# Kernel tuning notes

Hardware: AMD Instinct MI355X
Metric: run time of the kernel (lower is better)

The kernel has to match this reference:

```python
import jax, jax.numpy as jnp
import numpy as np

N_NODES = 10000
N_PAIRS = 200000
NUM_FEATURES = 384
DEGREES = [1, 2, 3]
NHEADS = len(DEGREES)
F_HEAD = NUM_FEATURES // NHEADS  # 128
REPEATS = np.array([2 * d + 1 for d in DEGREES])  # [3,5,7]
SPH_DIM = int(REPEATS.sum())  # 15


def setup_inputs() -> dict:
    key = jax.random.key(0)
    ks = jax.random.split(key, 10)
    return {
        "chi": jax.random.normal(ks[0], (N_NODES, SPH_DIM), dtype=jnp.float32),
        "sph_ij": jax.random.normal(ks[1], (N_PAIRS, SPH_DIM), dtype=jnp.float32),
        "x": jax.random.normal(ks[2], (N_NODES, NUM_FEATURES), dtype=jnp.float32),
        "w_ij": jax.random.normal(ks[3], (N_PAIRS, NUM_FEATURES), dtype=jnp.float32),
        "idx_i": jax.random.randint(ks[4], (N_PAIRS,), 0, N_NODES),
        "phi_r_cut": jax.random.uniform(ks[5], (N_PAIRS, 1), dtype=jnp.float32),
        "phi_chi_cut": jax.random.uniform(ks[6], (N_PAIRS,), dtype=jnp.float32),
        "idx_j": jax.random.randint(ks[7], (N_PAIRS,), 0, N_NODES),
        # per-head linear weights (nn.Linear stores (out, in); y = x @ W.T)
        "Wq": jax.random.normal(ks[8], (NHEADS, F_HEAD, F_HEAD), dtype=jnp.float32) / np.sqrt(F_HEAD),
        "Wk": jax.random.normal(ks[9], (NHEADS, F_HEAD, F_HEAD), dtype=jnp.float32) / np.sqrt(F_HEAD),
    }


def reference(chi, sph_ij, x, w_ij, idx_i, phi_r_cut, phi_chi_cut, idx_j, Wq, Wk):
    n = x.shape[0]
    # split into heads: (n, H, Fh) / (E, H, Fh)
    x_h = x.reshape(n, NHEADS, F_HEAD)
    w_h = w_ij.reshape(-1, NHEADS, F_HEAD)
    # per-head linears (vmapped Linear, no bias): y = x @ W.T
    q = jnp.einsum("nhf,hgf->nhg", x_h, Wq)  # (n, H, Fh)
    k = jnp.einsum("nhf,hgf->nhg", x_h, Wk)  # (n, H, Fh)
    # gather + elementwise attention coefficients per head: (E, H)
    alpha = (q[idx_i] * w_h * k[idx_j]).sum(-1) / np.sqrt(F_HEAD).astype(np.float32)
    # combine radial and sphc cutoffs
    alpha = alpha * phi_r_cut + alpha * phi_chi_cut[:, None]  # (E, H)
    # repeat each head over its 2l+1 spherical components -> (E, SPH_DIM)
    alpha_rep = jnp.repeat(alpha, REPEATS, axis=-1, total_repeat_length=SPH_DIM)
    # scatter-add messages into center atoms -> (n, SPH_DIM)
    chi_ = jax.ops.segment_sum(alpha_rep * sph_ij, idx_i, num_segments=n)
    return chi_
```

## Files before the change

kernel.cpp:

```cpp
#include <hip/hip_runtime.h>
#include <hip/hip_bf16.h>
#include <hip/hip_fp16.h>

#define N_NODES 10000
#define N_PAIRS 200000
#define NFEAT 384
#define FH 128
#define SPH 15

typedef __bf16 bf16x8 __attribute__((ext_vector_type(8)));
typedef _Float16 half8 __attribute__((ext_vector_type(8)));
typedef float f32x4 __attribute__((ext_vector_type(4)));

__device__ inline bf16x8 cvt8(const float* __restrict__ p) {
    float4 lo = *(const float4*)p;
    float4 hi = *(const float4*)(p + 4);
    bf16x8 r;
    r[0] = (__bf16)lo.x; r[1] = (__bf16)lo.y; r[2] = (__bf16)lo.z; r[3] = (__bf16)lo.w;
    r[4] = (__bf16)hi.x; r[5] = (__bf16)hi.y; r[6] = (__bf16)hi.z; r[7] = (__bf16)hi.w;
    return r;
}

__global__ __launch_bounds__(256) void qk_gemm_kernel(
        const float* __restrict__ x,
        const float* __restrict__ Wq,
        const float* __restrict__ Wk,
        _Float16* __restrict__ q, _Float16* __restrict__ k) {
    const int head = blockIdx.y;
    const int node0 = blockIdx.x * 16;
    const int wave = threadIdx.x >> 6;
    const int lane = threadIdx.x & 63;
    const int mrow = lane & 15;
    const int quad = lane >> 4;
    const float* xrow = x + (size_t)(node0 + mrow) * NFEAT + head * FH + quad * 8;
    bf16x8 afrag[4];
#pragma unroll
    for (int t = 0; t < 4; ++t) afrag[t] = cvt8(xrow + t * 32);

    for (int task = wave; task < 16; task += 4) {
        const int mat = task & 1;
        const int g0 = (task >> 1) * 16;
        const float* Wrow =
            (mat ? Wk : Wq) + (size_t)head * FH * FH + (size_t)(g0 + mrow) * FH + quad * 8;
        f32x4 acc = {0.f, 0.f, 0.f, 0.f};
#pragma unroll
        for (int t = 0; t < 4; ++t) {
            bf16x8 b = cvt8(Wrow + t * 32);
            acc = __builtin_amdgcn_mfma_f32_16x16x32_bf16(afrag[t], b, acc, 0, 0, 0);
        }
        _Float16* dst = mat ? k : q;
        const int g = g0 + mrow;
#pragma unroll
        for (int r = 0; r < 4; ++r) {
            const int node = node0 + quad * 4 + r;
            dst[(size_t)node * NFEAT + head * FH + g] = (_Float16)acc[r];
        }
    }
}

__global__ __launch_bounds__(256) void pair_kernel(
        const _Float16* __restrict__ q, const _Float16* __restrict__ kk,
        const float* __restrict__ w_ij, const float* __restrict__ sph,
        const int* __restrict__ idx_i, const int* __restrict__ idx_j,
        const float* __restrict__ phi_r, const float* __restrict__ phi_chi,
        float* __restrict__ out) {
    const int lane = threadIdx.x & 63;
    const int sub = lane & 15;
    const int grp = lane >> 4;
    const int wid = blockIdx.x * (blockDim.x >> 6) + (threadIdx.x >> 6);
    const int nw = gridDim.x * (blockDim.x >> 6);
    for (int base = wid * 4; base < N_PAIRS; base += nw * 4) {
        const int e = base + grp;
        if (e < N_PAIRS) {
            const int i = idx_i[e];
            const int j = idx_j[e];
            const _Float16* qr = q + (size_t)i * NFEAT;
            const _Float16* kr = kk + (size_t)j * NFEAT;
            const float* wr = w_ij + (size_t)e * NFEAT;
            float dot[3];
#pragma unroll
            for (int h = 0; h < 3; ++h) {
                const int f = h * FH + sub * 8;
                half8 qv = *(const half8*)(qr + f);
                half8 kv = *(const half8*)(kr + f);
                f32x4 wa = __builtin_nontemporal_load((const f32x4*)(wr + f));
                f32x4 wb = __builtin_nontemporal_load((const f32x4*)(wr + f + 4));
                float p = 0.f;
#pragma unroll
                for (int u = 0; u < 4; ++u) {
                    p = fmaf((float)qv[u] * wa[u], (float)kv[u], p);
                    p = fmaf((float)qv[u + 4] * wb[u], (float)kv[u + 4], p);
                }
#pragma unroll
                for (int off = 8; off; off >>= 1) p += __shfl_xor(p, off, 16);
                dot[h] = p;
            }
            const float pr = __builtin_nontemporal_load(phi_r + e);
            const float pc = __builtin_nontemporal_load(phi_chi + e);
            const float scale = (pr + pc) * 0.088388347648318447f;
            if (sub < SPH) {
                const int h = (sub < 3) ? 0 : (sub < 8 ? 1 : 2);
                const float s = __builtin_nontemporal_load(sph + (size_t)e * SPH + sub);
                const float val = dot[h] * scale * s;
                unsafeAtomicAdd(&out[(size_t)i * SPH + sub], val);
            }
        }
    }
}

extern "C" void kernel_launch(void* const* d_in, const int* in_sizes, int n_in,
                              void* d_out, int out_size, void* d_ws, size_t ws_size,
                              hipStream_t stream) {
    const float* sph     = (const float*)d_in[1];
    const float* x       = (const float*)d_in[2];
    const float* w_ij    = (const float*)d_in[3];
    const int*   idx_i   = (const int*)d_in[4];
    const float* phi_r   = (const float*)d_in[5];
    const float* phi_chi = (const float*)d_in[6];
    const int*   idx_j   = (const int*)d_in[7];
    const float* Wq      = (const float*)d_in[8];
    const float* Wk      = (const float*)d_in[9];
    float* out = (float*)d_out;

    char* ws = (char*)d_ws;
    _Float16* qws = (_Float16*)ws;
    _Float16* kws = (_Float16*)(ws + 7680000);

    hipMemsetAsync(d_out, 0, (size_t)out_size * sizeof(float), stream);

    qk_gemm_kernel<<<dim3(N_NODES / 16, 3), 256, 0, stream>>>(x, Wq, Wk, qws, kws);

    pair_kernel<<<2048, 256, 0, stream>>>(qws, kws, w_ij, sph, idx_i, idx_j,
                                          phi_r, phi_chi, out);
}
```

Measured before the change: 482.1 us.

## Pre-convert GEMM inputs to bf16, hoist pair loads, resize pair grid

```diff
diff --git a/kernel.cpp b/kernel.cpp
--- a/kernel.cpp
+++ b/kernel.cpp
@@ -9,22 +9,37 @@
 #define SPH 15
 
 typedef __bf16 bf16x8 __attribute__((ext_vector_type(8)));
+typedef __bf16 bf16x4 __attribute__((ext_vector_type(4)));
 typedef _Float16 half8 __attribute__((ext_vector_type(8)));
 typedef float f32x4 __attribute__((ext_vector_type(4)));
 
-__device__ inline bf16x8 cvt8(const float* __restrict__ p) {
-    float4 lo = *(const float4*)p;
-    float4 hi = *(const float4*)(p + 4);
-    bf16x8 r;
-    r[0] = (__bf16)lo.x; r[1] = (__bf16)lo.y; r[2] = (__bf16)lo.z; r[3] = (__bf16)lo.w;
-    r[4] = (__bf16)hi.x; r[5] = (__bf16)hi.y; r[6] = (__bf16)hi.z; r[7] = (__bf16)hi.w;
-    return r;
+__global__ __launch_bounds__(256) void cvt_kernel(
+        const float* __restrict__ x, const float* __restrict__ Wq,
+        const float* __restrict__ Wk, __bf16* __restrict__ xb,
+        __bf16* __restrict__ wqb, __bf16* __restrict__ wkb) {
+    const int XN4 = (N_NODES * NFEAT) / 4;
+    const int WN4 = (3 * FH * FH) / 4;
+    const int total = XN4 + 2 * WN4;
+    for (int t = blockIdx.x * blockDim.x + threadIdx.x; t < total;
+         t += gridDim.x * blockDim.x) {
+        const float* src;
+        __bf16* dst;
+        int o;
+        if (t < XN4)            { src = x;  dst = xb;  o = t; }
+        else if (t < XN4 + WN4) { src = Wq; dst = wqb; o = t - XN4; }
+        else                    { src = Wk; dst = wkb; o = t - XN4 - WN4; }
+        float4 v = *(const float4*)(src + (size_t)o * 4);
+        bf16x4 r;
+        r[0] = (__bf16)v.x; r[1] = (__bf16)v.y;
+        r[2] = (__bf16)v.z; r[3] = (__bf16)v.w;
+        *(bf16x4*)(dst + (size_t)o * 4) = r;
+    }
 }
 
 __global__ __launch_bounds__(256) void qk_gemm_kernel(
-        const float* __restrict__ x,
-        const float* __restrict__ Wq,
-        const float* __restrict__ Wk,
+        const __bf16* __restrict__ xb,
+        const __bf16* __restrict__ Wqb,
+        const __bf16* __restrict__ Wkb,
         _Float16* __restrict__ q, _Float16* __restrict__ k) {
     const int head = blockIdx.y;
     const int node0 = blockIdx.x * 16;
@@ -32,20 +47,20 @@
     const int lane = threadIdx.x & 63;
     const int mrow = lane & 15;
     const int quad = lane >> 4;
-    const float* xrow = x + (size_t)(node0 + mrow) * NFEAT + head * FH + quad * 8;
+    const __bf16* xrow = xb + (size_t)(node0 + mrow) * NFEAT + head * FH + quad * 8;
     bf16x8 afrag[4];
 #pragma unroll
-    for (int t = 0; t < 4; ++t) afrag[t] = cvt8(xrow + t * 32);
+    for (int t = 0; t < 4; ++t) afrag[t] = *(const bf16x8*)(xrow + t * 32);
 
     for (int task = wave; task < 16; task += 4) {
         const int mat = task & 1;
         const int g0 = (task >> 1) * 16;
-        const float* Wrow =
-            (mat ? Wk : Wq) + (size_t)head * FH * FH + (size_t)(g0 + mrow) * FH + quad * 8;
+        const __bf16* Wrow =
+            (mat ? Wkb : Wqb) + (size_t)head * FH * FH + (size_t)(g0 + mrow) * FH + quad * 8;
         f32x4 acc = {0.f, 0.f, 0.f, 0.f};
 #pragma unroll
         for (int t = 0; t < 4; ++t) {
-            bf16x8 b = cvt8(Wrow + t * 32);
+            bf16x8 b = *(const bf16x8*)(Wrow + t * 32);
             acc = __builtin_amdgcn_mfma_f32_16x16x32_bf16(afrag[t], b, acc, 0, 0, 0);
         }
         _Float16* dst = mat ? k : q;
@@ -71,39 +86,39 @@
     const int nw = gridDim.x * (blockDim.x >> 6);
     for (int base = wid * 4; base < N_PAIRS; base += nw * 4) {
         const int e = base + grp;
-        if (e < N_PAIRS) {
-            const int i = idx_i[e];
-            const int j = idx_j[e];
-            const _Float16* qr = q + (size_t)i * NFEAT;
-            const _Float16* kr = kk + (size_t)j * NFEAT;
-            const float* wr = w_ij + (size_t)e * NFEAT;
-            float dot[3];
+        const int i = idx_i[e];
+        const int j = idx_j[e];
+        const float pr = __builtin_nontemporal_load(phi_r + e);
+        const float pc = __builtin_nontemporal_load(phi_chi + e);
+        float sv = 0.f;
+        if (sub < SPH)
+            sv = __builtin_nontemporal_load(sph + (size_t)e * SPH + sub);
+        const _Float16* qr = q + (size_t)i * NFEAT;
+        const _Float16* kr = kk + (size_t)j * NFEAT;
+        const float* wr = w_ij + (size_t)e * NFEAT;
+        float dot[3];
 #pragma unroll
-            for (int h = 0; h < 3; ++h) {
-                const int f = h * FH + sub * 8;
-                half8 qv = *(const half8*)(qr + f);
-                half8 kv = *(const half8*)(kr + f);
-                f32x4 wa = __builtin_nontemporal_load((const f32x4*)(wr + f));
-                f32x4 wb = __builtin_nontemporal_load((const f32x4*)(wr + f + 4));
-                float p = 0.f;
+        for (int h = 0; h < 3; ++h) {
+            const int f = h * FH + sub * 8;
+            half8 qv = *(const half8*)(qr + f);
+            half8 kv = *(const half8*)(kr + f);
+            f32x4 wa = __builtin_nontemporal_load((const f32x4*)(wr + f));
+            f32x4 wb = __builtin_nontemporal_load((const f32x4*)(wr + f + 4));
+            float d = 0.f;
 #pragma unroll
-                for (int u = 0; u < 4; ++u) {
-                    p = fmaf((float)qv[u] * wa[u], (float)kv[u], p);
-                    p = fmaf((float)qv[u + 4] * wb[u], (float)kv[u + 4], p);
-                }
+            for (int u = 0; u < 4; ++u) {
+                d = fmaf((float)qv[u] * wa[u], (float)kv[u], d);
+                d = fmaf((float)qv[u + 4] * wb[u], (float)kv[u + 4], d);
+            }
 #pragma unroll
-                for (int off = 8; off; off >>= 1) p += __shfl_xor(p, off, 16);
-                dot[h] = p;
-            }
-            const float pr = __builtin_nontemporal_load(phi_r + e);
-            const float pc = __builtin_nontemporal_load(phi_chi + e);
-            const float scale = (pr + pc) * 0.088388347648318447f;
-            if (sub < SPH) {
-                const int h = (sub < 3) ? 0 : (sub < 8 ? 1 : 2);
-                const float s = __builtin_nontemporal_load(sph + (size_t)e * SPH + sub);
-                const float val = dot[h] * scale * s;
-                unsafeAtomicAdd(&out[(size_t)i * SPH + sub], val);
-            }
+            for (int off = 8; off; off >>= 1) d += __shfl_xor(d, off, 16);
+            dot[h] = d;
+        }
+        const float scale = (pr + pc) * 0.088388347648318447f;
+        if (sub < SPH) {
+            const int h = (sub < 3) ? 0 : (sub < 8 ? 1 : 2);
+            const float val = dot[h] * scale * sv;
+            unsafeAtomicAdd(&out[(size_t)i * SPH + sub], val);
         }
     }
 }
@@ -125,11 +140,16 @@
     char* ws = (char*)d_ws;
     _Float16* qws = (_Float16*)ws;
     _Float16* kws = (_Float16*)(ws + 7680000);
+    __bf16* xb  = (__bf16*)(ws + 15360000);
+    __bf16* wqb = (__bf16*)(ws + 23040000);
+    __bf16* wkb = (__bf16*)(ws + 23138304);
 
     hipMemsetAsync(d_out, 0, (size_t)out_size * sizeof(float), stream);
 
-    qk_gemm_kernel<<<dim3(N_NODES / 16, 3), 256, 0, stream>>>(x, Wq, Wk, qws, kws);
+    cvt_kernel<<<2048, 256, 0, stream>>>(x, Wq, Wk, xb, wqb, wkb);
 
-    pair_kernel<<<2048, 256, 0, stream>>>(qws, kws, w_ij, sph, idx_i, idx_j,
+    qk_gemm_kernel<<<dim3(N_NODES / 16, 3), 256, 0, stream>>>(xb, wqb, wkb, qws, kws);
+
+    pair_kernel<<<3125, 256, 0, stream>>>(qws, kws, w_ij, sph, idx_i, idx_j,
                                           phi_r, phi_chi, out);
 }
```

New measurement: 469.6 us. 2.6% less time.
